# Kernel tuning notes

Measured on AMD Instinct MI355X. Metric: run time of the kernel, lower is better.

The kernel has to match this reference:

```python
import jax, jax.numpy as jnp
import numpy as np


def bilinear_sampler(img, flow):
    """Warp img (B,H,W,C) by per-pixel flow (B,H,W,2): sample at (x+u, y+v).
    Border handling: indices clipped to the image (edge padding)."""
    B, H, W, C = img.shape
    gy, gx = jnp.meshgrid(jnp.arange(H, dtype=img.dtype),
                          jnp.arange(W, dtype=img.dtype), indexing='ij')
    x = gx[None] + flow[..., 0]  # (B,H,W)
    y = gy[None] + flow[..., 1]
    x0f = jnp.floor(x)
    y0f = jnp.floor(y)
    wx = x - x0f  # fractional parts, differentiable w.r.t. flow
    wy = y - y0f
    x0 = jnp.clip(x0f.astype(jnp.int32), 0, W - 1)
    x1 = jnp.clip(x0f.astype(jnp.int32) + 1, 0, W - 1)
    y0 = jnp.clip(y0f.astype(jnp.int32), 0, H - 1)
    y1 = jnp.clip(y0f.astype(jnp.int32) + 1, 0, H - 1)
    b = jnp.arange(B)[:, None, None]
    Ia = img[b, y0, x0]  # (B,H,W,C)
    Ib = img[b, y1, x0]
    Ic = img[b, y0, x1]
    Id = img[b, y1, x1]
    wx = wx[..., None]
    wy = wy[..., None]
    return (Ia * (1 - wx) * (1 - wy) + Ib * (1 - wx) * wy
            + Ic * wx * (1 - wy) + Id * wx * wy)


def setup_inputs() -> dict:
    key = jax.random.key(0)
    k1, k2, k3, k4, k5, k6 = jax.random.split(key, 6)
    B, H, W = 8, 512, 512
    return {
        't': jax.random.uniform(k1, (B, 1, 1, 1), dtype=jnp.float32),
        'I0': jax.random.uniform(k2, (B, H, W, 3), dtype=jnp.float32),
        'I1': jax.random.uniform(k3, (B, H, W, 3), dtype=jnp.float32),
        'interp': jax.random.normal(k4, (B, H, W, 5), dtype=jnp.float32),
        'Fhat_t0': jax.random.normal(k5, (B, H, W, 2), dtype=jnp.float32),
        'Fhat_t1': jax.random.normal(k6, (B, H, W, 2), dtype=jnp.float32),
    }


def reference(t, I0, I1, interp, Fhat_t0, Fhat_t1):
    Ft0 = interp[..., 0:2] + Fhat_t0
    Ft1 = interp[..., 2:4] + Fhat_t1
    Vt0 = jax.nn.sigmoid(interp[..., 4:5])  # (B,H,W,1) -> broadcasts over RGB
    Vt1 = 1.0 - Vt0
    g0 = bilinear_sampler(I0, Ft0)
    g1 = bilinear_sampler(I1, Ft1)
    eps = 1e-12
    w0 = (1.0 - t) * Vt0
    w1 = t * Vt1
    It = (w0 * g0 + w1 * g1) / (w0 + w1 + eps)
    return It
```

## Files before the change

### kernel.cpp

```cpp
#include <hip/hip_runtime.h>

constexpr int B_ = 8;
constexpr int H_ = 512;
constexpr int W_ = 512;
constexpr int HW_ = H_ * W_;
constexpr int NPIX = B_ * HW_;
constexpr int PPT = 2;
constexpr int NTHREADS_TOTAL = NPIX / PPT;

__device__ __forceinline__ void sample3(const float* __restrict__ img,
                                        float xx, float yy,
                                        float g[3]) {
    float x0f = floorf(xx);
    float y0f = floorf(yy);
    float wx = xx - x0f;
    float wy = yy - y0f;
    int ix = (int)x0f;
    int iy = (int)y0f;
    int x0 = min(max(ix, 0), W_ - 1);
    int x1 = min(max(ix + 1, 0), W_ - 1);
    int xb = min(max(ix, 0), W_ - 2);
    int y0 = min(max(iy, 0), H_ - 1);
    int y1 = min(max(iy + 1, 0), H_ - 1);

    float a[6], c[6];
    __builtin_memcpy(a, img + ((size_t)y0 * W_ + xb) * 3, 24);
    __builtin_memcpy(c, img + ((size_t)y1 * W_ + xb) * 3, 24);

    bool hi0 = (x0 != xb);
    bool hi1 = (x1 != xb);

    float w00 = (1.0f - wx) * (1.0f - wy);
    float w01 = wx * (1.0f - wy);
    float w10 = (1.0f - wx) * wy;
    float w11 = wx * wy;

    #pragma unroll
    for (int ch = 0; ch < 3; ++ch) {
        float p00 = hi0 ? a[3 + ch] : a[ch];
        float p01 = hi1 ? a[3 + ch] : a[ch];
        float p10 = hi0 ? c[3 + ch] : c[ch];
        float p11 = hi1 ? c[3 + ch] : c[ch];
        g[ch] = p00 * w00 + p01 * w01 + p10 * w10 + p11 * w11;
    }
}

__global__ __launch_bounds__(256) void frame_interp_kernel(
    const float* __restrict__ t,
    const float* __restrict__ I0,
    const float* __restrict__ I1,
    const float* __restrict__ interp,
    const float* __restrict__ F0,
    const float* __restrict__ F1,
    float* __restrict__ out)
{
    int tid = blockIdx.x * blockDim.x + threadIdx.x;
    if (tid >= NTHREADS_TOTAL) return;
    int p2 = tid * PPT;
    int b    = p2 >> 18;
    int prow = (p2 & (HW_ - 1)) >> 9;
    int pcol = p2 & (W_ - 1);

    float tb = t[b];

    float ibuf[10];
    __builtin_memcpy(ibuf, interp + (size_t)p2 * 5, 40);

    float fb0[4], fb1[4];
    __builtin_memcpy(fb0, F0 + (size_t)p2 * 2, 16);
    __builtin_memcpy(fb1, F1 + (size_t)p2 * 2, 16);

    const float* img0 = I0 + (size_t)b * HW_ * 3;
    const float* img1 = I1 + (size_t)b * HW_ * 3;

    float obuf[6];

    #pragma unroll
    for (int j = 0; j < PPT; ++j) {
        float ft0x = ibuf[j * 5 + 0] + fb0[j * 2 + 0];
        float ft0y = ibuf[j * 5 + 1] + fb0[j * 2 + 1];
        float ft1x = ibuf[j * 5 + 2] + fb1[j * 2 + 0];
        float ft1y = ibuf[j * 5 + 3] + fb1[j * 2 + 1];
        float vt0  = 1.0f / (1.0f + expf(-ibuf[j * 5 + 4]));

        float xP = (float)(pcol + j);
        float yP = (float)prow;

        float g0[3], g1[3];
        sample3(img0, xP + ft0x, yP + ft0y, g0);
        sample3(img1, xP + ft1x, yP + ft1y, g1);

        float w0 = (1.0f - tb) * vt0;
        float w1 = tb * (1.0f - vt0);
        float inv = 1.0f / (w0 + w1 + 1e-12f);

        obuf[j * 3 + 0] = (w0 * g0[0] + w1 * g1[0]) * inv;
        obuf[j * 3 + 1] = (w0 * g0[1] + w1 * g1[1]) * inv;
        obuf[j * 3 + 2] = (w0 * g0[2] + w1 * g1[2]) * inv;
    }

    __builtin_memcpy(out + (size_t)p2 * 3, obuf, 24);
}

extern "C" void kernel_launch(void* const* d_in, const int* in_sizes, int n_in,
                              void* d_out, int out_size, void* d_ws, size_t ws_size,
                              hipStream_t stream) {
    const float* t      = (const float*)d_in[0];
    const float* I0     = (const float*)d_in[1];
    const float* I1     = (const float*)d_in[2];
    const float* interp = (const float*)d_in[3];
    const float* F0     = (const float*)d_in[4];
    const float* F1     = (const float*)d_in[5];
    float* out = (float*)d_out;

    int threads = 256;
    int blocks = NTHREADS_TOTAL / threads;
    frame_interp_kernel<<<blocks, threads, 0, stream>>>(t, I0, I1, interp, F0, F1, out);
}
```

Measured before the change: 199.2 us.

## Stage haloed image tiles in LDS for bilinear warping with global fallback

```diff
diff --git a/kernel.cpp b/kernel.cpp
--- a/kernel.cpp
+++ b/kernel.cpp
@@ -4,48 +4,56 @@
 constexpr int H_ = 512;
 constexpr int W_ = 512;
 constexpr int HW_ = H_ * W_;
-constexpr int NPIX = B_ * HW_;
-constexpr int PPT = 2;
-constexpr int NTHREADS_TOTAL = NPIX / PPT;
 
-__device__ __forceinline__ void sample3(const float* __restrict__ img,
-                                        float xx, float yy,
-                                        float g[3]) {
-    float x0f = floorf(xx);
-    float y0f = floorf(yy);
-    float wx = xx - x0f;
-    float wy = yy - y0f;
-    int ix = (int)x0f;
-    int iy = (int)y0f;
+constexpr int TS = 32;
+constexpr int R_ = 8;
+constexpr int RS = TS + 2 * R_;
+constexpr int RROW = RS * 3;
+constexpr int NSPX = RS * RS;
+
+__device__ __forceinline__ void sampleT(const float* __restrict__ lds,
+                                        const float* __restrict__ img,
+                                        int gx0, int gy0,
+                                        float sx, float sy, float g[3]) {
+    float xf = floorf(sx), yf = floorf(sy);
+    float wx = sx - xf, wy = sy - yf;
+    int ix = (int)xf, iy = (int)yf;
     int x0 = min(max(ix, 0), W_ - 1);
     int x1 = min(max(ix + 1, 0), W_ - 1);
-    int xb = min(max(ix, 0), W_ - 2);
     int y0 = min(max(iy, 0), H_ - 1);
     int y1 = min(max(iy + 1, 0), H_ - 1);
-
-    float a[6], c[6];
-    __builtin_memcpy(a, img + ((size_t)y0 * W_ + xb) * 3, 24);
-    __builtin_memcpy(c, img + ((size_t)y1 * W_ + xb) * 3, 24);
-
-    bool hi0 = (x0 != xb);
-    bool hi1 = (x1 != xb);
 
     float w00 = (1.0f - wx) * (1.0f - wy);
     float w01 = wx * (1.0f - wy);
     float w10 = (1.0f - wx) * wy;
     float w11 = wx * wy;
 
-    #pragma unroll
-    for (int ch = 0; ch < 3; ++ch) {
-        float p00 = hi0 ? a[3 + ch] : a[ch];
-        float p01 = hi1 ? a[3 + ch] : a[ch];
-        float p10 = hi0 ? c[3 + ch] : c[ch];
-        float p11 = hi1 ? c[3 + ch] : c[ch];
-        g[ch] = p00 * w00 + p01 * w01 + p10 * w10 + p11 * w11;
+    int lx0 = x0 - gx0, lx1 = x1 - gx0;
+    int ly0 = y0 - gy0, ly1 = y1 - gy0;
+    bool inT = ((unsigned)lx0 < (unsigned)RS) & ((unsigned)lx1 < (unsigned)RS) &
+               ((unsigned)ly0 < (unsigned)RS) & ((unsigned)ly1 < (unsigned)RS);
+
+    if (inT) {
+        const float* a = lds + ly0 * RROW;
+        const float* c = lds + ly1 * RROW;
+        int o0 = lx0 * 3, o1 = lx1 * 3;
+        #pragma unroll
+        for (int ch = 0; ch < 3; ++ch)
+            g[ch] = a[o0 + ch] * w00 + a[o1 + ch] * w01 +
+                    c[o0 + ch] * w10 + c[o1 + ch] * w11;
+    } else {
+        const float* pa = img + ((size_t)y0 * W_ + x0) * 3;
+        const float* pb = img + ((size_t)y0 * W_ + x1) * 3;
+        const float* pc = img + ((size_t)y1 * W_ + x0) * 3;
+        const float* pd = img + ((size_t)y1 * W_ + x1) * 3;
+        #pragma unroll
+        for (int ch = 0; ch < 3; ++ch)
+            g[ch] = pa[ch] * w00 + pb[ch] * w01 +
+                    pc[ch] * w10 + pd[ch] * w11;
     }
 }
 
-__global__ __launch_bounds__(256) void frame_interp_kernel(
+__global__ __launch_bounds__(256) void frame_interp_tiled(
     const float* __restrict__ t,
     const float* __restrict__ I0,
     const float* __restrict__ I1,
@@ -54,52 +62,74 @@
     const float* __restrict__ F1,
     float* __restrict__ out)
 {
-    int tid = blockIdx.x * blockDim.x + threadIdx.x;
-    if (tid >= NTHREADS_TOTAL) return;
-    int p2 = tid * PPT;
-    int b    = p2 >> 18;
-    int prow = (p2 & (HW_ - 1)) >> 9;
-    int pcol = p2 & (W_ - 1);
+    __shared__ float lds0[RS * RROW];
+    __shared__ float lds1[RS * RROW];
 
-    float tb = t[b];
-
-    float ibuf[10];
-    __builtin_memcpy(ibuf, interp + (size_t)p2 * 5, 40);
-
-    float fb0[4], fb1[4];
-    __builtin_memcpy(fb0, F0 + (size_t)p2 * 2, 16);
-    __builtin_memcpy(fb1, F1 + (size_t)p2 * 2, 16);
+    int tid = threadIdx.x;
+    int bid = blockIdx.x;
+    int b    = bid & 7;
+    int tile = bid >> 3;
+    int ty   = tile >> 4;
+    int tx   = tile & 15;
+    int gx0 = tx * TS - R_;
+    int gy0 = ty * TS - R_;
 
     const float* img0 = I0 + (size_t)b * HW_ * 3;
     const float* img1 = I1 + (size_t)b * HW_ * 3;
 
-    float obuf[6];
+    #pragma unroll
+    for (int k = 0; k < NSPX / 256; ++k) {
+        int p  = tid + k * 256;
+        int ry = p / RS;
+        int pu = p - ry * RS;
+        int gy = min(max(gy0 + ry, 0), H_ - 1);
+        int gx = min(max(gx0 + pu, 0), W_ - 1);
+        size_t s = ((size_t)gy * W_ + gx) * 3;
+        int d = p * 3;
+        lds0[d + 0] = img0[s + 0];
+        lds0[d + 1] = img0[s + 1];
+        lds0[d + 2] = img0[s + 2];
+        lds1[d + 0] = img1[s + 0];
+        lds1[d + 1] = img1[s + 1];
+        lds1[d + 2] = img1[s + 2];
+    }
+    __syncthreads();
+
+    float tb = t[b];
 
     #pragma unroll
-    for (int j = 0; j < PPT; ++j) {
-        float ft0x = ibuf[j * 5 + 0] + fb0[j * 2 + 0];
-        float ft0y = ibuf[j * 5 + 1] + fb0[j * 2 + 1];
-        float ft1x = ibuf[j * 5 + 2] + fb1[j * 2 + 0];
-        float ft1y = ibuf[j * 5 + 3] + fb1[j * 2 + 1];
-        float vt0  = 1.0f / (1.0f + expf(-ibuf[j * 5 + 4]));
+    for (int k = 0; k < 4; ++k) {
+        int p   = tid + k * 256;
+        int row = p >> 5;
+        int col = p & 31;
+        int gx = tx * TS + col;
+        int gy = ty * TS + row;
+        int idx = b * HW_ + gy * W_ + gx;
 
-        float xP = (float)(pcol + j);
-        float yP = (float)prow;
+        const float* ip  = interp + (size_t)idx * 5;
+        float i0 = ip[0], i1 = ip[1], i2 = ip[2], i3 = ip[3], i4 = ip[4];
+        const float* f0p = F0 + (size_t)idx * 2;
+        const float* f1p = F1 + (size_t)idx * 2;
+
+        float ft0x = i0 + f0p[0];
+        float ft0y = i1 + f0p[1];
+        float ft1x = i2 + f1p[0];
+        float ft1y = i3 + f1p[1];
+        float vt0  = 1.0f / (1.0f + __expf(-i4));
 
         float g0[3], g1[3];
-        sample3(img0, xP + ft0x, yP + ft0y, g0);
-        sample3(img1, xP + ft1x, yP + ft1y, g1);
+        sampleT(lds0, img0, gx0, gy0, (float)gx + ft0x, (float)gy + ft0y, g0);
+        sampleT(lds1, img1, gx0, gy0, (float)gx + ft1x, (float)gy + ft1y, g1);
 
         float w0 = (1.0f - tb) * vt0;
         float w1 = tb * (1.0f - vt0);
         float inv = 1.0f / (w0 + w1 + 1e-12f);
 
-        obuf[j * 3 + 0] = (w0 * g0[0] + w1 * g1[0]) * inv;
-        obuf[j * 3 + 1] = (w0 * g0[1] + w1 * g1[1]) * inv;
-        obuf[j * 3 + 2] = (w0 * g0[2] + w1 * g1[2]) * inv;
+        float* op = out + (size_t)idx * 3;
+        op[0] = (w0 * g0[0] + w1 * g1[0]) * inv;
+        op[1] = (w0 * g0[1] + w1 * g1[1]) * inv;
+        op[2] = (w0 * g0[2] + w1 * g1[2]) * inv;
     }
-
-    __builtin_memcpy(out + (size_t)p2 * 3, obuf, 24);
 }
 
 extern "C" void kernel_launch(void* const* d_in, const int* in_sizes, int n_in,
@@ -113,7 +143,6 @@
     const float* F1     = (const float*)d_in[5];
     float* out = (float*)d_out;
 
-    int threads = 256;
-    int blocks = NTHREADS_TOTAL / threads;
-    frame_interp_kernel<<<blocks, threads, 0, stream>>>(t, I0, I1, interp, F0, F1, out);
+    int blocks = B_ * (H_ / TS) * (W_ / TS);
+    frame_interp_tiled<<<blocks, 256, 0, stream>>>(t, I0, I1, interp, F0, F1, out);
 }
```

After: 164.9 us. 17.2% less time.

## Pre-convert images to padded fp16 RGBX and gather with half2 math

Applied to the files above, without the earlier changes.

```diff
diff --git a/kernel.cpp b/kernel.cpp
--- a/kernel.cpp
+++ b/kernel.cpp
@@ -1,105 +1,173 @@
 #include <hip/hip_runtime.h>
+#include <hip/hip_fp16.h>
 
 constexpr int B_ = 8;
 constexpr int H_ = 512;
 constexpr int W_ = 512;
 constexpr int HW_ = H_ * W_;
 constexpr int NPIX = B_ * HW_;
-constexpr int PPT = 2;
-constexpr int NTHREADS_TOTAL = NPIX / PPT;
 
-__device__ __forceinline__ void sample3(const float* __restrict__ img,
-                                        float xx, float yy,
-                                        float g[3]) {
-    float x0f = floorf(xx);
-    float y0f = floorf(yy);
-    float wx = xx - x0f;
-    float wy = yy - y0f;
-    int ix = (int)x0f;
-    int iy = (int)y0f;
+__device__ __forceinline__ unsigned h2u(__half2 h) { unsigned u; __builtin_memcpy(&u, &h, 4); return u; }
+__device__ __forceinline__ __half2 u2h(unsigned u) { __half2 h; __builtin_memcpy(&h, &u, 4); return h; }
+
+__global__ __launch_bounds__(256) void convert_rgbx(
+    const float* __restrict__ I0, const float* __restrict__ I1,
+    uint2* __restrict__ H0, uint2* __restrict__ H1)
+{
+    int bid   = blockIdx.x;
+    int b     = bid & 7;
+    int img   = (bid >> 3) & 1;
+    int chunk = bid >> 4;
+    const float* src = (img ? I1 : I0) + (size_t)b * HW_ * 3;
+    uint2*       dst = (img ? H1 : H0) + (size_t)b * HW_;
+    int p0 = chunk * 1024 + threadIdx.x * 4;
+    float c[12];
+    __builtin_memcpy(c, src + (size_t)p0 * 3, 48);
+    uint2 o[4];
+    #pragma unroll
+    for (int j = 0; j < 4; ++j) {
+        __half2 rg = __floats2half2_rn(c[j * 3 + 0], c[j * 3 + 1]);
+        __half2 bx = __floats2half2_rn(c[j * 3 + 2], 0.0f);
+        o[j].x = h2u(rg);
+        o[j].y = h2u(bx);
+    }
+    __builtin_memcpy(dst + p0, o, 32);
+}
+
+__device__ __forceinline__ void sampleH(const uint2* __restrict__ img,
+                                        float sx, float sy, float g[3]) {
+    float xf = floorf(sx), yf = floorf(sy);
+    float wx = sx - xf, wy = sy - yf;
+    int ix = (int)xf, iy = (int)yf;
     int x0 = min(max(ix, 0), W_ - 1);
     int x1 = min(max(ix + 1, 0), W_ - 1);
     int xb = min(max(ix, 0), W_ - 2);
     int y0 = min(max(iy, 0), H_ - 1);
     int y1 = min(max(iy + 1, 0), H_ - 1);
 
-    float a[6], c[6];
-    __builtin_memcpy(a, img + ((size_t)y0 * W_ + xb) * 3, 24);
-    __builtin_memcpy(c, img + ((size_t)y1 * W_ + xb) * 3, 24);
+    uint4 ra, rc;
+    __builtin_memcpy(&ra, img + (size_t)y0 * W_ + xb, 16);
+    __builtin_memcpy(&rc, img + (size_t)y1 * W_ + xb, 16);
 
     bool hi0 = (x0 != xb);
     bool hi1 = (x1 != xb);
 
-    float w00 = (1.0f - wx) * (1.0f - wy);
-    float w01 = wx * (1.0f - wy);
-    float w10 = (1.0f - wx) * wy;
-    float w11 = wx * wy;
+    unsigned a_rg0 = hi0 ? ra.z : ra.x, a_b0 = hi0 ? ra.w : ra.y;
+    unsigned a_rg1 = hi1 ? ra.z : ra.x, a_b1 = hi1 ? ra.w : ra.y;
+    unsigned c_rg0 = hi0 ? rc.z : rc.x, c_b0 = hi0 ? rc.w : rc.y;
+    unsigned c_rg1 = hi1 ? rc.z : rc.x, c_b1 = hi1 ? rc.w : rc.y;
 
-    #pragma unroll
-    for (int ch = 0; ch < 3; ++ch) {
-        float p00 = hi0 ? a[3 + ch] : a[ch];
-        float p01 = hi1 ? a[3 + ch] : a[ch];
-        float p10 = hi0 ? c[3 + ch] : c[ch];
-        float p11 = hi1 ? c[3 + ch] : c[ch];
-        g[ch] = p00 * w00 + p01 * w01 + p10 * w10 + p11 * w11;
-    }
+    __half2 h00 = __float2half2_rn((1.0f - wx) * (1.0f - wy));
+    __half2 h01 = __float2half2_rn(wx * (1.0f - wy));
+    __half2 h10 = __float2half2_rn((1.0f - wx) * wy);
+    __half2 h11 = __float2half2_rn(wx * wy);
+
+    __half2 rg = __hmul2(h00, u2h(a_rg0));
+    rg = __hfma2(h01, u2h(a_rg1), rg);
+    rg = __hfma2(h10, u2h(c_rg0), rg);
+    rg = __hfma2(h11, u2h(c_rg1), rg);
+    __half2 bb = __hmul2(h00, u2h(a_b0));
+    bb = __hfma2(h01, u2h(a_b1), bb);
+    bb = __hfma2(h10, u2h(c_b0), bb);
+    bb = __hfma2(h11, u2h(c_b1), bb);
+
+    g[0] = __low2float(rg);
+    g[1] = __high2float(rg);
+    g[2] = __low2float(bb);
 }
 
-__global__ __launch_bounds__(256) void frame_interp_kernel(
+__global__ __launch_bounds__(256) void frame_interp_gather(
     const float* __restrict__ t,
-    const float* __restrict__ I0,
-    const float* __restrict__ I1,
     const float* __restrict__ interp,
     const float* __restrict__ F0,
     const float* __restrict__ F1,
+    const uint2* __restrict__ H0,
+    const uint2* __restrict__ H1,
     float* __restrict__ out)
 {
-    int tid = blockIdx.x * blockDim.x + threadIdx.x;
-    if (tid >= NTHREADS_TOTAL) return;
-    int p2 = tid * PPT;
-    int b    = p2 >> 18;
-    int prow = (p2 & (HW_ - 1)) >> 9;
-    int pcol = p2 & (W_ - 1);
+    int bid  = blockIdx.x;
+    int b    = bid & 7;
+    int row  = bid >> 3;
+    int idx  = b * HW_ + row * W_ + (int)threadIdx.x * 2;
+
+    float ib[10];
+    __builtin_memcpy(ib, interp + (size_t)idx * 5, 40);
+    float f0[4], f1[4];
+    __builtin_memcpy(f0, F0 + (size_t)idx * 2, 16);
+    __builtin_memcpy(f1, F1 + (size_t)idx * 2, 16);
 
     float tb = t[b];
+    const uint2* h0 = H0 + (size_t)b * HW_;
+    const uint2* h1 = H1 + (size_t)b * HW_;
 
-    float ibuf[10];
-    __builtin_memcpy(ibuf, interp + (size_t)p2 * 5, 40);
-
-    float fb0[4], fb1[4];
-    __builtin_memcpy(fb0, F0 + (size_t)p2 * 2, 16);
-    __builtin_memcpy(fb1, F1 + (size_t)p2 * 2, 16);
-
-    const float* img0 = I0 + (size_t)b * HW_ * 3;
-    const float* img1 = I1 + (size_t)b * HW_ * 3;
-
-    float obuf[6];
-
+    float o[6];
     #pragma unroll
-    for (int j = 0; j < PPT; ++j) {
-        float ft0x = ibuf[j * 5 + 0] + fb0[j * 2 + 0];
-        float ft0y = ibuf[j * 5 + 1] + fb0[j * 2 + 1];
-        float ft1x = ibuf[j * 5 + 2] + fb1[j * 2 + 0];
-        float ft1y = ibuf[j * 5 + 3] + fb1[j * 2 + 1];
-        float vt0  = 1.0f / (1.0f + expf(-ibuf[j * 5 + 4]));
-
-        float xP = (float)(pcol + j);
-        float yP = (float)prow;
+    for (int j = 0; j < 2; ++j) {
+        float x = (float)((int)threadIdx.x * 2 + j);
+        float y = (float)row;
+        float ft0x = ib[j * 5 + 0] + f0[j * 2 + 0];
+        float ft0y = ib[j * 5 + 1] + f0[j * 2 + 1];
+        float ft1x = ib[j * 5 + 2] + f1[j * 2 + 0];
+        float ft1y = ib[j * 5 + 3] + f1[j * 2 + 1];
+        float vt0  = 1.0f / (1.0f + __expf(-ib[j * 5 + 4]));
 
         float g0[3], g1[3];
-        sample3(img0, xP + ft0x, yP + ft0y, g0);
-        sample3(img1, xP + ft1x, yP + ft1y, g1);
+        sampleH(h0, x + ft0x, y + ft0y, g0);
+        sampleH(h1, x + ft1x, y + ft1y, g1);
 
         float w0 = (1.0f - tb) * vt0;
         float w1 = tb * (1.0f - vt0);
         float inv = 1.0f / (w0 + w1 + 1e-12f);
+        o[j * 3 + 0] = (w0 * g0[0] + w1 * g1[0]) * inv;
+        o[j * 3 + 1] = (w0 * g0[1] + w1 * g1[1]) * inv;
+        o[j * 3 + 2] = (w0 * g0[2] + w1 * g1[2]) * inv;
+    }
+    __builtin_memcpy(out + (size_t)idx * 3, o, 24);
+}
 
-        obuf[j * 3 + 0] = (w0 * g0[0] + w1 * g1[0]) * inv;
-        obuf[j * 3 + 1] = (w0 * g0[1] + w1 * g1[1]) * inv;
-        obuf[j * 3 + 2] = (w0 * g0[2] + w1 * g1[2]) * inv;
+__global__ __launch_bounds__(256) void frame_interp_naive(
+    const float* __restrict__ t,  const float* __restrict__ I0,
+    const float* __restrict__ I1, const float* __restrict__ interp,
+    const float* __restrict__ F0, const float* __restrict__ F1,
+    float* __restrict__ out)
+{
+    int idx = blockIdx.x * blockDim.x + threadIdx.x;
+    if (idx >= NPIX) return;
+    int b = idx >> 18;
+    int p = idx & (HW_ - 1);
+    int y = p >> 9;
+    int x = p & (W_ - 1);
+    const float* ip = interp + (size_t)idx * 5;
+    float2 f0 = *(const float2*)(F0 + (size_t)idx * 2);
+    float2 f1 = *(const float2*)(F1 + (size_t)idx * 2);
+    float tb = t[b];
+    float vt0 = 1.0f / (1.0f + __expf(-ip[4]));
+    const float* img[2] = { I0 + (size_t)b * HW_ * 3, I1 + (size_t)b * HW_ * 3 };
+    float sx[2] = { x + ip[0] + f0.x, x + ip[2] + f1.x };
+    float sy[2] = { y + ip[1] + f0.y, y + ip[3] + f1.y };
+    float g[2][3];
+    #pragma unroll
+    for (int s = 0; s < 2; ++s) {
+        float xf = floorf(sx[s]), yf = floorf(sy[s]);
+        float wx = sx[s] - xf, wy = sy[s] - yf;
+        int x0 = min(max((int)xf, 0), W_ - 1);
+        int x1 = min(max((int)xf + 1, 0), W_ - 1);
+        int y0 = min(max((int)yf, 0), H_ - 1);
+        int y1 = min(max((int)yf + 1, 0), H_ - 1);
+        const float* pa = img[s] + ((size_t)y0 * W_ + x0) * 3;
+        const float* pb = img[s] + ((size_t)y1 * W_ + x0) * 3;
+        const float* pc = img[s] + ((size_t)y0 * W_ + x1) * 3;
+        const float* pd = img[s] + ((size_t)y1 * W_ + x1) * 3;
+        #pragma unroll
+        for (int ch = 0; ch < 3; ++ch)
+            g[s][ch] = pa[ch] * (1 - wx) * (1 - wy) + pb[ch] * (1 - wx) * wy
+                     + pc[ch] * wx * (1 - wy) + pd[ch] * wx * wy;
     }
-
-    __builtin_memcpy(out + (size_t)p2 * 3, obuf, 24);
+    float w0 = (1.0f - tb) * vt0, w1 = tb * (1.0f - vt0);
+    float inv = 1.0f / (w0 + w1 + 1e-12f);
+    float* op = out + (size_t)idx * 3;
+    #pragma unroll
+    for (int ch = 0; ch < 3; ++ch) op[ch] = (w0 * g[0][ch] + w1 * g[1][ch]) * inv;
 }
 
 extern "C" void kernel_launch(void* const* d_in, const int* in_sizes, int n_in,
@@ -113,7 +181,14 @@
     const float* F1     = (const float*)d_in[5];
     float* out = (float*)d_out;
 
-    int threads = 256;
-    int blocks = NTHREADS_TOTAL / threads;
-    frame_interp_kernel<<<blocks, threads, 0, stream>>>(t, I0, I1, interp, F0, F1, out);
+    size_t need = (size_t)2 * NPIX * sizeof(uint2);
+    if (ws_size >= need) {
+        uint2* H0 = (uint2*)d_ws;
+        uint2* H1 = H0 + NPIX;
+        convert_rgbx<<<4096, 256, 0, stream>>>(I0, I1, H0, H1);
+        frame_interp_gather<<<4096, 256, 0, stream>>>(t, interp, F0, F1, H0, H1, out);
+    } else {
+        frame_interp_naive<<<(NPIX + 255) / 256, 256, 0, stream>>>(
+            t, I0, I1, interp, F0, F1, out);
+    }
 }
```

Measured after the change: 185.2 us. 7.0% less time.
